# Kernel optimization log

Hardware: AMD Instinct MI355X
Metric: run time of the kernel (lower is better)

## Reference

```python
import jax, jax.numpy as jnp
import numpy as np

B, C, H, W = 2, 128, 48, 48
NUM_HEADS = 8


def dct_matrix(N):
    # Orthonormal DCT-II matrix: D[k, n] = s_k * cos(pi * (n + 0.5) * k / N)
    n = np.arange(N)
    D = np.cos(np.pi * (n[None, :] + 0.5) * n[:, None] / N) * np.sqrt(2.0 / N)
    D[0] *= 1.0 / np.sqrt(2.0)
    return jnp.asarray(D, dtype=jnp.float32)


def setup_inputs() -> dict:
    key = jax.random.key(0)
    ks = jax.random.split(key, 10)
    w_scale = 1.0 / np.sqrt(C)  # kaiming-ish init for 1x1 convs
    inp = {
        "freq_feat": jax.random.normal(ks[0], (B, C, H, W), dtype=jnp.float32),
        "spatial_feat": jax.random.normal(ks[1], (B, C, H, W), dtype=jnp.float32),
        "Wq": jax.random.normal(ks[2], (C, C), dtype=jnp.float32) * w_scale,
        "bq": jnp.zeros((C,), dtype=jnp.float32),
        "Wk": jax.random.normal(ks[3], (C, C), dtype=jnp.float32) * w_scale,
        "bk": jnp.zeros((C,), dtype=jnp.float32),
        "Wv": jax.random.normal(ks[4], (C, C), dtype=jnp.float32) * w_scale,
        "bv": jnp.zeros((C,), dtype=jnp.float32),
        "Wo": jax.random.normal(ks[5], (C, C), dtype=jnp.float32) * w_scale,
        "bo": jnp.zeros((C,), dtype=jnp.float32),
    }
    return inp


def _proj(x, Wm, b):
    # 1x1 conv == channel-mixing GEMM
    return jnp.einsum('oc,bchw->bohw', Wm, x) + b[None, :, None, None]


def reference(freq_feat, spatial_feat, Wq, bq, Wk, bk, Wv, bv, Wo, bo):
    b, c, h, w = freq_feat.shape
    nh = NUM_HEADS
    d = c // nh
    L = h * w

    # 2D orthonormal DCT-II of the spatial features
    DH = dct_matrix(h)
    DW = dct_matrix(w)
    spatial_freq = jnp.einsum('hm,bcmn,wn->bchw', DH, spatial_feat, DW)

    Q = _proj(freq_feat, Wq, bq)
    K = _proj(spatial_freq, Wk, bk)
    V = _proj(spatial_freq, Wv, bv)

    # (B, C, H, W) -> (B, nh, L, d)
    def to_heads(x):
        return x.reshape(b, nh, d, L).transpose(0, 1, 3, 2)

    Qh, Kh, Vh = to_heads(Q), to_heads(K), to_heads(V)

    scale = 1.0 / np.sqrt(d)
    scores = jnp.einsum('bhld,bhsd->bhls', Qh, Kh) * scale  # (B, nh, L, L)
    attn = jax.nn.softmax(scores, axis=-1)
    out = jnp.einsum('bhls,bhsd->bhld', attn, Vh)  # (B, nh, L, d)

    out = out.transpose(0, 1, 3, 2).reshape(b, c, h, w)
    return _proj(out, Wo, bo)
```

## Files before the change

kernel.cpp:

```cpp
#include <hip/hip_runtime.h>
#include <math.h>

#define L_TOT 2304
#define C_TOT 128
#define KSCALE 0.36067376022224085f

#if __has_builtin(__builtin_amdgcn_exp2f)
#define EXP2(x) __builtin_amdgcn_exp2f(x)
#else
#define EXP2(x) __expf(0.69314718055994531f * (x))
#endif

typedef float v4f  __attribute__((ext_vector_type(4)));
typedef __bf16 v8bf __attribute__((ext_vector_type(8)));
typedef __bf16 v4bf __attribute__((ext_vector_type(4)));

#define MFMA_16x16x32_BF16(A, B, C) __builtin_amdgcn_mfma_f32_16x16x32_bf16((A), (B), (C), 0, 0, 0)

__device__ __forceinline__ void async_cp16(const __bf16* g, __bf16* l){
  __builtin_amdgcn_global_load_lds((const __attribute__((address_space(1))) unsigned int*)g,
                                   (__attribute__((address_space(3))) unsigned int*)l,
                                   16, 0, 0);
}

template<int MODE>
__device__ __forceinline__ void mfma_proj(const float* __restrict__ W,
                                          const float* __restrict__ bias,
                                          const float* __restrict__ Xb,
                                          __bf16* __restrict__ Yh,
                                          float scale, float bscale,
                                          int n0, __bf16* Bhi, int tid){
  __bf16* Blo = Bhi + 4352;
  const int wave = tid >> 6, lane = tid & 63, qd = lane >> 4, cn = lane & 15;
  const int m0 = wave * 32;
  v8bf ahi[2][4], alo[2][4];
  #pragma unroll
  for (int rt = 0; rt < 2; rt++)
    #pragma unroll
    for (int ks = 0; ks < 4; ks++){
      const float* wp = W + (size_t)(m0 + rt * 16 + cn) * C_TOT + ks * 32 + qd * 8;
      float4 w0 = *(const float4*)wp;
      float4 w1 = *(const float4*)(wp + 4);
      float wv[8] = {w0.x, w0.y, w0.z, w0.w, w1.x, w1.y, w1.z, w1.w};
      #pragma unroll
      for (int j = 0; j < 8; j++){
        __bf16 h = (__bf16)wv[j];
        ahi[rt][ks][j] = h;
        alo[rt][ks][j] = (__bf16)(wv[j] - (float)h);
      }
    }
  {
    int k = tid >> 1, nh = tid & 1;
    const float* xp = Xb + (size_t)k * L_TOT + n0 + nh * 16;
    float4 x0 = *(const float4*)xp;
    float4 x1 = *(const float4*)(xp + 4);
    float4 x2 = *(const float4*)(xp + 8);
    float4 x3 = *(const float4*)(xp + 12);
    float xv[16] = {x0.x, x0.y, x0.z, x0.w, x1.x, x1.y, x1.z, x1.w,
                    x2.x, x2.y, x2.z, x2.w, x3.x, x3.y, x3.z, x3.w};
    #pragma unroll
    for (int i = 0; i < 16; i++){
      __bf16 h = (__bf16)xv[i];
      int row = nh * 16 + i;
      Bhi[row * 136 + k] = h;
      Blo[row * 136 + k] = (__bf16)(xv[i] - (float)h);
    }
  }
  __syncthreads();
  v4f acc[2][2];
  #pragma unroll
  for (int rt = 0; rt < 2; rt++)
    #pragma unroll
    for (int ct = 0; ct < 2; ct++) acc[rt][ct] = (v4f){0.f, 0.f, 0.f, 0.f};
  #pragma unroll
  for (int ks = 0; ks < 4; ks++){
    v8bf bhi[2], blo[2];
    #pragma unroll
    for (int ct = 0; ct < 2; ct++){
      bhi[ct] = *(const v8bf*)&Bhi[(ct * 16 + cn) * 136 + ks * 32 + qd * 8];
      blo[ct] = *(const v8bf*)&Blo[(ct * 16 + cn) * 136 + ks * 32 + qd * 8];
    }
    #pragma unroll
    for (int rt = 0; rt < 2; rt++)
      #pragma unroll
      for (int ct = 0; ct < 2; ct++){
        acc[rt][ct] = MFMA_16x16x32_BF16(ahi[rt][ks], bhi[ct], acc[rt][ct]);
        acc[rt][ct] = MFMA_16x16x32_BF16(ahi[rt][ks], blo[ct], acc[rt][ct]);
        acc[rt][ct] = MFMA_16x16x32_BF16(alo[rt][ks], bhi[ct], acc[rt][ct]);
      }
  }
  #pragma unroll
  for (int rt = 0; rt < 2; rt++){
    float bv[4];
    #pragma unroll
    for (int r = 0; r < 4; r++) bv[r] = bias[m0 + rt * 16 + qd * 4 + r] * bscale;
    #pragma unroll
    for (int ct = 0; ct < 2; ct++){
      int col = n0 + ct * 16 + cn;
      if (MODE == 1){
        v4bf kk;
        #pragma unroll
        for (int r = 0; r < 4; r++) kk[r] = (__bf16)((acc[rt][ct][r] + bv[r]) * scale);
        *(v4bf*)&Yh[(size_t)col * C_TOT + m0 + rt * 16 + qd * 4] = kk;
      } else {
        #pragma unroll
        for (int r = 0; r < 4; r++)
          Yh[(size_t)(m0 + rt * 16 + qd * 4 + r) * L_TOT + col] = (__bf16)(acc[rt][ct][r] + bv[r]);
      }
    }
  }
}

__global__ __launch_bounds__(256) void k_qkv(
    const float* __restrict__ freq, const float* __restrict__ spat,
    const float* __restrict__ Wq, const float* __restrict__ bq,
    const float* __restrict__ Wk, const float* __restrict__ bk,
    const float* __restrict__ Wv, const float* __restrict__ bv,
    __bf16* __restrict__ QT, __bf16* __restrict__ Kraw, __bf16* __restrict__ Vraw){
  __shared__ __align__(16) unsigned char smraw[17408];
  int job = blockIdx.x / 144;
  int idx = blockIdx.x % 144;
  int b = idx / 72, n0 = (idx % 72) * 32;
  size_t off = (size_t)b * C_TOT * L_TOT;
  if (job == 0)
    mfma_proj<1>(Wq, bq, freq + off, QT + (size_t)b * L_TOT * C_TOT, 1.0f, 1.0f, n0, (__bf16*)smraw, threadIdx.x);
  else if (job == 1)
    mfma_proj<2>(Wk, bk, spat + off, Kraw + off, 1.0f, 0.0f, n0, (__bf16*)smraw, threadIdx.x);
  else
    mfma_proj<2>(Wv, bv, spat + off, Vraw + off, 1.0f, 0.0f, n0, (__bf16*)smraw, threadIdx.x);
}

__global__ __launch_bounds__(256) void k_dct_kv(const __bf16* __restrict__ Kraw,
                                                const __bf16* __restrict__ Vraw,
                                                const float* __restrict__ bk,
                                                const float* __restrict__ bv,
                                                __bf16* __restrict__ KT,
                                                __bf16* __restrict__ Vg){
  __shared__ __align__(16) __bf16 Xs[3456];
  __shared__ __align__(16) __bf16 Dm[3456];
  __shared__ __align__(16) __bf16 Tt[3456];
  int blk = blockIdx.x, tid = threadIdx.x;
  int isV = blk >> 8;
  int img = blk & 255;
  int b = img >> 7, c = img & 127;
  const __bf16* src = (isV ? Vraw : Kraw) + (size_t)img * 2304;
  float bias = (isV ? bv : bk)[c];
  for (int i = tid; i < 1728; i += 256){
    ((unsigned int*)Xs)[i] = 0u;
    ((unsigned int*)Dm)[i] = 0u;
    ((unsigned int*)Tt)[i] = 0u;
  }
  __syncthreads();
  for (int i = tid; i < 2304; i += 256){
    int a = i / 48, n = i - a * 48;
    int m = ((2 * n + 1) * a) % 192;
    float v = cosf(0.032724923474893679f * (float)m) * 0.204124145231931508f;
    if (a == 0) v *= 0.707106781186547524f;
    Dm[a * 72 + n] = (__bf16)v;
  }
  for (int t = tid; t < 288; t += 256){
    int m = t / 6, j = t - m * 6;
    *(v8bf*)&Xs[m * 72 + j * 8] = *(const v8bf*)(src + t * 8);
  }
  __syncthreads();
  int wave = tid >> 6, lane = tid & 63, qd = lane >> 4, cn = lane & 15;
  for (int t = wave; t < 9; t += 4){
    int mi = t / 3, wi = t - mi * 3;
    v8bf a0 = *(const v8bf*)&Xs[(mi * 16 + cn) * 72 + qd * 8];
    v8bf a1 = *(const v8bf*)&Xs[(mi * 16 + cn) * 72 + 32 + qd * 8];
    v8bf b0 = *(const v8bf*)&Dm[(wi * 16 + cn) * 72 + qd * 8];
    v8bf b1 = *(const v8bf*)&Dm[(wi * 16 + cn) * 72 + 32 + qd * 8];
    v4f acc = (v4f){0.f, 0.f, 0.f, 0.f};
    acc = MFMA_16x16x32_BF16(a0, b0, acc);
    acc = MFMA_16x16x32_BF16(a1, b1, acc);
    v4bf w4;
    #pragma unroll
    for (int r = 0; r < 4; r++) w4[r] = (__bf16)acc[r];
    *(v4bf*)&Tt[(wi * 16 + cn) * 72 + mi * 16 + qd * 4] = w4;
  }
  __syncthreads();
  for (int t = wave; t < 9; t += 4){
    int hi = t / 3, wi = t - hi * 3;
    v8bf a0 = *(const v8bf*)&Dm[(hi * 16 + cn) * 72 + qd * 8];
    v8bf a1 = *(const v8bf*)&Dm[(hi * 16 + cn) * 72 + 32 + qd * 8];
    v8bf b0 = *(const v8bf*)&Tt[(wi * 16 + cn) * 72 + qd * 8];
    v8bf b1 = *(const v8bf*)&Tt[(wi * 16 + cn) * 72 + 32 + qd * 8];
    v4f acc = (v4f){0.f, 0.f, 0.f, 0.f};
    acc = MFMA_16x16x32_BF16(a0, b0, acc);
    acc = MFMA_16x16x32_BF16(a1, b1, acc);
    int w = wi * 16 + cn;
    if (!isV){
      #pragma unroll
      for (int r = 0; r < 4; r++){
        int l = (hi * 16 + qd * 4 + r) * 48 + w;
        KT[((size_t)b * L_TOT + l) * C_TOT + c] = (__bf16)((acc[r] + bias) * KSCALE);
      }
    } else {
      #pragma unroll
      for (int r = 0; r < 4; r++){
        int l = (hi * 16 + qd * 4 + r) * 48 + w;
        Vg[(size_t)img * 2304 + l] = (__bf16)(acc[r] + bias);
      }
    }
  }
}

__global__ __launch_bounds__(256) void k_attn(const __bf16* __restrict__ QT,
                                              const __bf16* __restrict__ KT,
                                              const __bf16* __restrict__ V,
                                              __bf16* __restrict__ AO){
  const int L = L_TOT;
  int bh = blockIdx.y;
  int b = bh >> 3, h = bh & 7;
  int c0 = h * 16;
  const __bf16* QTb = QT + (size_t)b * L * C_TOT;
  const __bf16* KTb = KT + (size_t)b * L * C_TOT;
  const __bf16* Vb  = V  + ((size_t)b * C_TOT + c0) * L;
  int tid = threadIdx.x;
  int wave = tid >> 6, lane = tid & 63;
  int qd = lane >> 4, cn = lane & 15;
  int l0 = blockIdx.x * 48;

  __shared__ __align__(16) __bf16 smem[8192 + 8192 + 7680];
  __bf16* Kt = smem;
  __bf16* Vs = smem + 8192;
  __bf16* Pt = smem + 16384;

  v8bf qf[3];
  #pragma unroll
  for (int t = 0; t < 3; t++){
    #pragma unroll
    for (int j = 0; j < 8; j++) qf[t][j] = (__bf16)0.0f;
  }
  if (qd < 2){
    #pragma unroll
    for (int t = 0; t < 3; t++)
      qf[t] = *(const v8bf*)&QTb[(size_t)(l0 + t * 16 + cn) * C_TOT + c0 + qd * 8];
  }

  v4f acc[3];
  float den[3] = {0.f, 0.f, 0.f};
  #pragma unroll
  for (int t = 0; t < 3; t++) acc[t] = (v4f){0.f, 0.f, 0.f, 0.f};

  for (int ch = 0; ch < 5; ch++){
    int s0 = ch * 512;
    int cnt = (ch == 4) ? 256 : 512;
    __syncthreads();
    {
      int per = (cnt >> 5) >> 2;
      for (int jj = 0; jj < per; jj++){
        int j = wave * per + jj;
        int s = j * 32 + (lane >> 1);
        async_cp16(KTb + (size_t)(s0 + s) * C_TOT + c0 + (lane & 1) * 8,
                   Kt + j * 512);
      }
      if (cnt == 512){
        #pragma unroll
        for (int jj = 0; jj < 4; jj++){
          int d = wave * 4 + jj;
          async_cp16(Vb + (size_t)d * L + s0 + ((lane ^ (d & 7)) << 3),
                     Vs + d * 512);
        }
      } else {
        int d = tid >> 4, og = tid & 15;
        const __bf16* gp = Vb + (size_t)d * L + s0 + og * 16;
        v8bf v0 = *(const v8bf*)gp;
        v8bf v1 = *(const v8bf*)(gp + 8);
        int pd = d & 7;
        *(v8bf*)&Vs[d * 512 + (((og * 2)     ^ pd) << 3)] = v0;
        *(v8bf*)&Vs[d * 512 + (((og * 2 + 1) ^ pd) << 3)] = v1;
      }
    }
    __syncthreads();

    int nsu = cnt >> 7;
    int wbase = wave * (cnt >> 2);
    for (int su = 0; su < nsu; su++){
      int sb = wbase + su * 32;
      v8bf a0, a1;
      #pragma unroll
      for (int j = 0; j < 8; j++){ a0[j] = (__bf16)0.0f; a1[j] = (__bf16)0.0f; }
      if (qd < 2){
        a0 = *(const v8bf*)&Kt[(sb + cn) * 16 + qd * 8];
        a1 = *(const v8bf*)&Kt[(sb + 16 + cn) * 16 + qd * 8];
      }
      int jv = sb >> 3;
      v8bf vf = *(const v8bf*)&Vs[cn * 512 + (((jv + qd) ^ (cn & 7)) << 3)];
      #pragma unroll
      for (int t = 0; t < 3; t++){
        v4f z = {0.f, 0.f, 0.f, 0.f};
        v4f st0 = MFMA_16x16x32_BF16(a0, qf[t], z);
        v4f st1 = MFMA_16x16x32_BF16(a1, qf[t], z);
        float p0[4], p1[4];
        #pragma unroll
        for (int i = 0; i < 4; i++){
          p0[i] = EXP2(st0[i]); den[t] += p0[i];
          p1[i] = EXP2(st1[i]); den[t] += p1[i];
        }
        v4bf w0, w1;
        #pragma unroll
        for (int i = 0; i < 4; i++){ w0[i] = (__bf16)p0[i]; w1[i] = (__bf16)p1[i]; }
        __bf16* Ptw = Pt + (wave * 3 + t) * 640;
        *(v4bf*)&Ptw[cn * 40 + qd * 4]      = w0;
        *(v4bf*)&Ptw[cn * 40 + 16 + qd * 4] = w1;
        v8bf pf = *(const v8bf*)&Ptw[cn * 40 + qd * 8];
        acc[t] = MFMA_16x16x32_BF16(vf, pf, acc[t]);
      }
    }
  }

  __syncthreads();
  float* redA = (float*)smem;
  float* redD = (float*)smem + 3072;
  #pragma unroll
  for (int t = 0; t < 3; t++){
    *(v4f*)&redA[((wave * 3 + t) * 64 + lane) * 4] = acc[t];
    redD[(wave * 3 + t) * 64 + lane] = den[t];
  }
  __syncthreads();
  if (wave < 3){
    int t = wave;
    v4f a = (v4f){0.f, 0.f, 0.f, 0.f};
    float dn = 0.f;
    #pragma unroll
    for (int w2 = 0; w2 < 4; w2++){
      v4f xx = *(const v4f*)&redA[((w2 * 3 + t) * 64 + lane) * 4];
      a[0] += xx[0]; a[1] += xx[1]; a[2] += xx[2]; a[3] += xx[3];
      dn += redD[(w2 * 3 + t) * 64 + lane];
    }
    dn += __shfl_xor(dn, 16);
    dn += __shfl_xor(dn, 32);
    float inv = 1.0f / dn;
    __bf16* Ao = AO + ((size_t)b * C_TOT + c0) * L;
    #pragma unroll
    for (int r2 = 0; r2 < 4; r2++)
      Ao[(size_t)(qd * 4 + r2) * L + l0 + t * 16 + cn] = (__bf16)(a[r2] * inv);
  }
}

__global__ __launch_bounds__(256) void k_oproj(const __bf16* __restrict__ AO,
                                               const float* __restrict__ Wo, const float* __restrict__ bo,
                                               float* __restrict__ out){
  __shared__ __align__(16) __bf16 Bs[32 * 136];
  int b = blockIdx.y, n0 = blockIdx.x * 32;
  int tid = threadIdx.x;
  const int wave = tid >> 6, lane = tid & 63, qd = lane >> 4, cn = lane & 15;
  const int m0 = wave * 32;
  v8bf ahi[2][4], alo[2][4];
  #pragma unroll
  for (int rt = 0; rt < 2; rt++)
    #pragma unroll
    for (int ks = 0; ks < 4; ks++){
      const float* wp = Wo + (size_t)(m0 + rt * 16 + cn) * C_TOT + ks * 32 + qd * 8;
      float4 w0 = *(const float4*)wp;
      float4 w1 = *(const float4*)(wp + 4);
      float wv[8] = {w0.x, w0.y, w0.z, w0.w, w1.x, w1.y, w1.z, w1.w};
      #pragma unroll
      for (int j = 0; j < 8; j++){
        __bf16 h = (__bf16)wv[j];
        ahi[rt][ks][j] = h;
        alo[rt][ks][j] = (__bf16)(wv[j] - (float)h);
      }
    }
  {
    int k = tid >> 1, nh = tid & 1;
    const __bf16* src = AO + ((size_t)b * C_TOT + k) * L_TOT + n0 + nh * 16;
    v8bf x0 = *(const v8bf*)src;
    v8bf x1 = *(const v8bf*)(src + 8);
    #pragma unroll
    for (int i = 0; i < 8; i++){
      Bs[(nh * 16 + i) * 136 + k] = x0[i];
      Bs[(nh * 16 + 8 + i) * 136 + k] = x1[i];
    }
  }
  __syncthreads();
  v4f acc[2][2];
  #pragma unroll
  for (int rt = 0; rt < 2; rt++)
    #pragma unroll
    for (int ct = 0; ct < 2; ct++) acc[rt][ct] = (v4f){0.f, 0.f, 0.f, 0.f};
  #pragma unroll
  for (int ks = 0; ks < 4; ks++){
    v8bf bf[2];
    #pragma unroll
    for (int ct = 0; ct < 2; ct++)
      bf[ct] = *(const v8bf*)&Bs[(ct * 16 + cn) * 136 + ks * 32 + qd * 8];
    #pragma unroll
    for (int rt = 0; rt < 2; rt++)
      #pragma unroll
      for (int ct = 0; ct < 2; ct++){
        acc[rt][ct] = MFMA_16x16x32_BF16(ahi[rt][ks], bf[ct], acc[rt][ct]);
        acc[rt][ct] = MFMA_16x16x32_BF16(alo[rt][ks], bf[ct], acc[rt][ct]);
      }
  }
  float* ob = out + (size_t)b * C_TOT * L_TOT;
  #pragma unroll
  for (int rt = 0; rt < 2; rt++){
    float bv[4];
    #pragma unroll
    for (int r = 0; r < 4; r++) bv[r] = bo[m0 + rt * 16 + qd * 4 + r];
    #pragma unroll
    for (int ct = 0; ct < 2; ct++){
      int col = n0 + ct * 16 + cn;
      #pragma unroll
      for (int r = 0; r < 4; r++)
        ob[(size_t)(m0 + rt * 16 + qd * 4 + r) * L_TOT + col] = acc[rt][ct][r] + bv[r];
    }
  }
}

extern "C" void kernel_launch(void* const* d_in, const int* in_sizes, int n_in,
                              void* d_out, int out_size, void* d_ws, size_t ws_size,
                              hipStream_t stream){
  const float* freq = (const float*)d_in[0];
  const float* spat = (const float*)d_in[1];
  const float* Wq = (const float*)d_in[2]; const float* bq = (const float*)d_in[3];
  const float* Wk = (const float*)d_in[4]; const float* bk = (const float*)d_in[5];
  const float* Wv = (const float*)d_in[6]; const float* bv = (const float*)d_in[7];
  const float* Wo = (const float*)d_in[8]; const float* bo = (const float*)d_in[9];
  __bf16* base = (__bf16*)d_ws;

  __bf16* QTg  = base;
  __bf16* Kraw = base + 589824;
  __bf16* Vraw = base + 1179648;
  __bf16* KTg  = base + 1769472;
  __bf16* Vg   = base + 2359296;
  __bf16* AOg  = base + 2949120;
  float* out = (float*)d_out;

  k_qkv<<<dim3(432), dim3(256), 0, stream>>>(freq, spat, Wq, bq, Wk, bk, Wv, bv,
                                             QTg, Kraw, Vraw);
  k_dct_kv<<<dim3(512), dim3(256), 0, stream>>>(Kraw, Vraw, bk, bv, KTg, Vg);
  k_attn<<<dim3(48, 16), dim3(256), 0, stream>>>(QTg, KTg, Vg, AOg);
  k_oproj<<<dim3(72, 2), dim3(256), 0, stream>>>(AOg, Wo, bo, out);
}
```

Before: 116.9 us.

## Apply DCT before K/V projections and use permlane swaps for P fragments

Reorders the pipeline so the 2D DCT runs once per spatial channel image, using split bf16 hi/lo MFMAs and writing fp32 results, before the K and V projections, instead of transforming the projected K and V separately. This halves the DCT work and removes the strided per-channel KT scatter, at the cost of an fp32 intermediate buffer. Separately, the attention kernel now rearranges the softmax P tile for the PV MFMA with v_permlane32/16_swap instead of a round trip through LDS, which frees 15 KB of shared memory per block.

New measurement: 115.8 us. No clear change (-1.0%).

```diff
diff --git a/kernel.cpp b/kernel.cpp
--- a/kernel.cpp
+++ b/kernel.cpp
@@ -22,6 +22,27 @@
                                    (__attribute__((address_space(3))) unsigned int*)l,
                                    16, 0, 0);
 }
+
+#if __has_builtin(__builtin_amdgcn_permlane32_swap)
+__device__ __forceinline__ void pl32swap(unsigned &a, unsigned &b){
+  auto r = __builtin_amdgcn_permlane32_swap((int)a, (int)b, false, false);
+  a = (unsigned)r[0]; b = (unsigned)r[1];
+}
+#else
+__device__ __forceinline__ void pl32swap(unsigned &a, unsigned &b){
+  asm volatile("v_permlane32_swap_b32 %0, %1" : "+v"(a), "+v"(b));
+}
+#endif
+#if __has_builtin(__builtin_amdgcn_permlane16_swap)
+__device__ __forceinline__ void pl16swap(unsigned &a, unsigned &b){
+  auto r = __builtin_amdgcn_permlane16_swap((int)a, (int)b, false, false);
+  a = (unsigned)r[0]; b = (unsigned)r[1];
+}
+#else
+__device__ __forceinline__ void pl16swap(unsigned &a, unsigned &b){
+  asm volatile("v_permlane16_swap_b32 %0, %1" : "+v"(a), "+v"(b));
+}
+#endif
 
 template<int MODE>
 __device__ __forceinline__ void mfma_proj(const float* __restrict__ W,
@@ -111,98 +132,103 @@
   }
 }
 
-__global__ __launch_bounds__(256) void k_qkv(
+__global__ __launch_bounds__(256) void k_q_dct(
     const float* __restrict__ freq, const float* __restrict__ spat,
     const float* __restrict__ Wq, const float* __restrict__ bq,
+    __bf16* __restrict__ QT, float* __restrict__ SF){
+  __shared__ __align__(16) unsigned char smraw[34560];
+  int tid = threadIdx.x;
+  if (blockIdx.x < 144){
+    int idx = blockIdx.x;
+    int b = idx / 72, n0 = (idx % 72) * 32;
+    size_t off = (size_t)b * C_TOT * L_TOT;
+    mfma_proj<1>(Wq, bq, freq + off, QT + (size_t)b * L_TOT * C_TOT, 1.0f, 1.0f, n0, (__bf16*)smraw, tid);
+    return;
+  }
+  int img = blockIdx.x - 144;
+  __bf16* Xhi = (__bf16*)smraw;
+  __bf16* Xlo = Xhi + 3456;
+  __bf16* Dm  = Xhi + 6912;
+  __bf16* Thi = Xhi + 10368;
+  __bf16* Tlo = Xhi + 13824;
+  const float* src = spat + (size_t)img * 2304;
+  for (int i = tid; i < 8640; i += 256) ((unsigned int*)smraw)[i] = 0u;
+  __syncthreads();
+  for (int i = tid; i < 2304; i += 256){
+    int a = i / 48, n = i - a * 48;
+    int m = ((2 * n + 1) * a) % 192;
+    float v = cosf(0.032724923474893679f * (float)m) * 0.204124145231931508f;
+    if (a == 0) v *= 0.707106781186547524f;
+    Dm[a * 72 + n] = (__bf16)v;
+  }
+  for (int i = tid; i < 2304; i += 256){
+    int mm = i / 48, n = i - mm * 48;
+    float v = src[i];
+    __bf16 h = (__bf16)v;
+    Xhi[mm * 72 + n] = h;
+    Xlo[mm * 72 + n] = (__bf16)(v - (float)h);
+  }
+  __syncthreads();
+  int wave = tid >> 6, lane = tid & 63, qd = lane >> 4, cn = lane & 15;
+  for (int t = wave; t < 9; t += 4){
+    int mi = t / 3, wi = t - mi * 3;
+    v8bf ah0 = *(const v8bf*)&Xhi[(mi * 16 + cn) * 72 + qd * 8];
+    v8bf ah1 = *(const v8bf*)&Xhi[(mi * 16 + cn) * 72 + 32 + qd * 8];
+    v8bf al0 = *(const v8bf*)&Xlo[(mi * 16 + cn) * 72 + qd * 8];
+    v8bf al1 = *(const v8bf*)&Xlo[(mi * 16 + cn) * 72 + 32 + qd * 8];
+    v8bf b0 = *(const v8bf*)&Dm[(wi * 16 + cn) * 72 + qd * 8];
+    v8bf b1 = *(const v8bf*)&Dm[(wi * 16 + cn) * 72 + 32 + qd * 8];
+    v4f acc = (v4f){0.f, 0.f, 0.f, 0.f};
+    acc = MFMA_16x16x32_BF16(ah0, b0, acc);
+    acc = MFMA_16x16x32_BF16(ah1, b1, acc);
+    acc = MFMA_16x16x32_BF16(al0, b0, acc);
+    acc = MFMA_16x16x32_BF16(al1, b1, acc);
+    v4bf th, tl;
+    #pragma unroll
+    for (int r = 0; r < 4; r++){
+      __bf16 h = (__bf16)acc[r];
+      th[r] = h;
+      tl[r] = (__bf16)(acc[r] - (float)h);
+    }
+    *(v4bf*)&Thi[(wi * 16 + cn) * 72 + mi * 16 + qd * 4] = th;
+    *(v4bf*)&Tlo[(wi * 16 + cn) * 72 + mi * 16 + qd * 4] = tl;
+  }
+  __syncthreads();
+  float* dst = SF + (size_t)img * 2304;
+  for (int t = wave; t < 9; t += 4){
+    int hi_ = t / 3, wi = t - hi_ * 3;
+    v8bf a0 = *(const v8bf*)&Dm[(hi_ * 16 + cn) * 72 + qd * 8];
+    v8bf a1 = *(const v8bf*)&Dm[(hi_ * 16 + cn) * 72 + 32 + qd * 8];
+    v8bf bh0 = *(const v8bf*)&Thi[(wi * 16 + cn) * 72 + qd * 8];
+    v8bf bh1 = *(const v8bf*)&Thi[(wi * 16 + cn) * 72 + 32 + qd * 8];
+    v8bf bl0 = *(const v8bf*)&Tlo[(wi * 16 + cn) * 72 + qd * 8];
+    v8bf bl1 = *(const v8bf*)&Tlo[(wi * 16 + cn) * 72 + 32 + qd * 8];
+    v4f acc = (v4f){0.f, 0.f, 0.f, 0.f};
+    acc = MFMA_16x16x32_BF16(a0, bh0, acc);
+    acc = MFMA_16x16x32_BF16(a1, bh1, acc);
+    acc = MFMA_16x16x32_BF16(a0, bl0, acc);
+    acc = MFMA_16x16x32_BF16(a1, bl1, acc);
+    int w = wi * 16 + cn;
+    #pragma unroll
+    for (int r = 0; r < 4; r++)
+      dst[(size_t)(hi_ * 16 + qd * 4 + r) * 48 + w] = acc[r];
+  }
+}
+
+__global__ __launch_bounds__(256) void k_kv(
+    const float* __restrict__ SF,
     const float* __restrict__ Wk, const float* __restrict__ bk,
     const float* __restrict__ Wv, const float* __restrict__ bv,
-    __bf16* __restrict__ QT, __bf16* __restrict__ Kraw, __bf16* __restrict__ Vraw){
+    __bf16* __restrict__ KT, __bf16* __restrict__ Vg){
   __shared__ __align__(16) unsigned char smraw[17408];
   int job = blockIdx.x / 144;
   int idx = blockIdx.x % 144;
   int b = idx / 72, n0 = (idx % 72) * 32;
   size_t off = (size_t)b * C_TOT * L_TOT;
   if (job == 0)
-    mfma_proj<1>(Wq, bq, freq + off, QT + (size_t)b * L_TOT * C_TOT, 1.0f, 1.0f, n0, (__bf16*)smraw, threadIdx.x);
-  else if (job == 1)
-    mfma_proj<2>(Wk, bk, spat + off, Kraw + off, 1.0f, 0.0f, n0, (__bf16*)smraw, threadIdx.x);
+    mfma_proj<1>(Wk, bk, SF + off, KT + (size_t)b * L_TOT * C_TOT, KSCALE, 1.0f, n0, (__bf16*)smraw, threadIdx.x);
   else
-    mfma_proj<2>(Wv, bv, spat + off, Vraw + off, 1.0f, 0.0f, n0, (__bf16*)smraw, threadIdx.x);
-}
-
-__global__ __launch_bounds__(256) void k_dct_kv(const __bf16* __restrict__ Kraw,
-                                                const __bf16* __restrict__ Vraw,
-                                                const float* __restrict__ bk,
-                                                const float* __restrict__ bv,
-                                                __bf16* __restrict__ KT,
-                                                __bf16* __restrict__ Vg){
-  __shared__ __align__(16) __bf16 Xs[3456];
-  __shared__ __align__(16) __bf16 Dm[3456];
-  __shared__ __align__(16) __bf16 Tt[3456];
-  int blk = blockIdx.x, tid = threadIdx.x;
-  int isV = blk >> 8;
-  int img = blk & 255;
-  int b = img >> 7, c = img & 127;
-  const __bf16* src = (isV ? Vraw : Kraw) + (size_t)img * 2304;
-  float bias = (isV ? bv : bk)[c];
-  for (int i = tid; i < 1728; i += 256){
-    ((unsigned int*)Xs)[i] = 0u;
-    ((unsigned int*)Dm)[i] = 0u;
-    ((unsigned int*)Tt)[i] = 0u;
-  }
-  __syncthreads();
-  for (int i = tid; i < 2304; i += 256){
-    int a = i / 48, n = i - a * 48;
-    int m = ((2 * n + 1) * a) % 192;
-    float v = cosf(0.032724923474893679f * (float)m) * 0.204124145231931508f;
-    if (a == 0) v *= 0.707106781186547524f;
-    Dm[a * 72 + n] = (__bf16)v;
-  }
-  for (int t = tid; t < 288; t += 256){
-    int m = t / 6, j = t - m * 6;
-    *(v8bf*)&Xs[m * 72 + j * 8] = *(const v8bf*)(src + t * 8);
-  }
-  __syncthreads();
-  int wave = tid >> 6, lane = tid & 63, qd = lane >> 4, cn = lane & 15;
-  for (int t = wave; t < 9; t += 4){
-    int mi = t / 3, wi = t - mi * 3;
-    v8bf a0 = *(const v8bf*)&Xs[(mi * 16 + cn) * 72 + qd * 8];
-    v8bf a1 = *(const v8bf*)&Xs[(mi * 16 + cn) * 72 + 32 + qd * 8];
-    v8bf b0 = *(const v8bf*)&Dm[(wi * 16 + cn) * 72 + qd * 8];
-    v8bf b1 = *(const v8bf*)&Dm[(wi * 16 + cn) * 72 + 32 + qd * 8];
-    v4f acc = (v4f){0.f, 0.f, 0.f, 0.f};
-    acc = MFMA_16x16x32_BF16(a0, b0, acc);
-    acc = MFMA_16x16x32_BF16(a1, b1, acc);
-    v4bf w4;
-    #pragma unroll
-    for (int r = 0; r < 4; r++) w4[r] = (__bf16)acc[r];
-    *(v4bf*)&Tt[(wi * 16 + cn) * 72 + mi * 16 + qd * 4] = w4;
-  }
-  __syncthreads();
-  for (int t = wave; t < 9; t += 4){
-    int hi = t / 3, wi = t - hi * 3;
-    v8bf a0 = *(const v8bf*)&Dm[(hi * 16 + cn) * 72 + qd * 8];
-    v8bf a1 = *(const v8bf*)&Dm[(hi * 16 + cn) * 72 + 32 + qd * 8];
-    v8bf b0 = *(const v8bf*)&Tt[(wi * 16 + cn) * 72 + qd * 8];
-    v8bf b1 = *(const v8bf*)&Tt[(wi * 16 + cn) * 72 + 32 + qd * 8];
-    v4f acc = (v4f){0.f, 0.f, 0.f, 0.f};
-    acc = MFMA_16x16x32_BF16(a0, b0, acc);
-    acc = MFMA_16x16x32_BF16(a1, b1, acc);
-    int w = wi * 16 + cn;
-    if (!isV){
-      #pragma unroll
-      for (int r = 0; r < 4; r++){
-        int l = (hi * 16 + qd * 4 + r) * 48 + w;
-        KT[((size_t)b * L_TOT + l) * C_TOT + c] = (__bf16)((acc[r] + bias) * KSCALE);
-      }
-    } else {
-      #pragma unroll
-      for (int r = 0; r < 4; r++){
-        int l = (hi * 16 + qd * 4 + r) * 48 + w;
-        Vg[(size_t)img * 2304 + l] = (__bf16)(acc[r] + bias);
-      }
-    }
-  }
+    mfma_proj<2>(Wv, bv, SF + off, Vg + off, 1.0f, 1.0f, n0, (__bf16*)smraw, threadIdx.x);
 }
 
 __global__ __launch_bounds__(256) void k_attn(const __bf16* __restrict__ QT,
@@ -221,10 +247,9 @@
   int qd = lane >> 4, cn = lane & 15;
   int l0 = blockIdx.x * 48;
 
-  __shared__ __align__(16) __bf16 smem[8192 + 8192 + 7680];
+  __shared__ __align__(16) __bf16 smem[8192 + 8192];
   __bf16* Kt = smem;
   __bf16* Vs = smem + 8192;
-  __bf16* Pt = smem + 16384;
 
   v8bf qf[3];
   #pragma unroll
@@ -298,13 +323,16 @@
           p0[i] = EXP2(st0[i]); den[t] += p0[i];
           p1[i] = EXP2(st1[i]); den[t] += p1[i];
         }
-        v4bf w0, w1;
+        v4bf cc0, cc1;
         #pragma unroll
-        for (int i = 0; i < 4; i++){ w0[i] = (__bf16)p0[i]; w1[i] = (__bf16)p1[i]; }
-        __bf16* Ptw = Pt + (wave * 3 + t) * 640;
-        *(v4bf*)&Ptw[cn * 40 + qd * 4]      = w0;
-        *(v4bf*)&Ptw[cn * 40 + 16 + qd * 4] = w1;
-        v8bf pf = *(const v8bf*)&Ptw[cn * 40 + qd * 8];
+        for (int i = 0; i < 4; i++){ cc0[i] = (__bf16)p0[i]; cc1[i] = (__bf16)p1[i]; }
+        unsigned U0 = ((unsigned*)&cc0)[0], U1 = ((unsigned*)&cc0)[1];
+        unsigned U2 = ((unsigned*)&cc1)[0], U3 = ((unsigned*)&cc1)[1];
+        pl32swap(U0, U2); pl32swap(U1, U3);
+        pl16swap(U0, U2); pl16swap(U1, U3);
+        v8bf pf;
+        ((unsigned*)&pf)[0] = U0; ((unsigned*)&pf)[1] = U1;
+        ((unsigned*)&pf)[2] = U2; ((unsigned*)&pf)[3] = U3;
         acc[t] = MFMA_16x16x32_BF16(vf, pf, acc[t]);
       }
     }
@@ -421,17 +449,15 @@
   const float* Wo = (const float*)d_in[8]; const float* bo = (const float*)d_in[9];
   __bf16* base = (__bf16*)d_ws;
 
-  __bf16* QTg  = base;
-  __bf16* Kraw = base + 589824;
-  __bf16* Vraw = base + 1179648;
-  __bf16* KTg  = base + 1769472;
-  __bf16* Vg   = base + 2359296;
-  __bf16* AOg  = base + 2949120;
+  __bf16* QTg = base;
+  __bf16* KTg = base + 589824;
+  __bf16* Vg  = base + 1179648;
+  __bf16* AOg = base + 1769472;
+  float*  SFg = (float*)(base + 2359296);
   float* out = (float*)d_out;
 
-  k_qkv<<<dim3(432), dim3(256), 0, stream>>>(freq, spat, Wq, bq, Wk, bk, Wv, bv,
-                                             QTg, Kraw, Vraw);
-  k_dct_kv<<<dim3(512), dim3(256), 0, stream>>>(Kraw, Vraw, bk, bv, KTg, Vg);
+  k_q_dct<<<dim3(400), dim3(256), 0, stream>>>(freq, spat, Wq, bq, QTg, SFg);
+  k_kv<<<dim3(288), dim3(256), 0, stream>>>(SFg, Wk, bk, Wv, bv, KTg, Vg);
   k_attn<<<dim3(48, 16), dim3(256), 0, stream>>>(QTg, KTg, Vg, AOg);
   k_oproj<<<dim3(72, 2), dim3(256), 0, stream>>>(AOg, Wo, bo, out);
 }
```
